# Optimization experiments

Hardware: AMD Instinct MI355X
Metric: run time of the kernel (lower is better)

## Reference

```python
import jax, jax.numpy as jnp
import numpy as np

P_SIZES = (1, 2, 4)
O_SIZE = 32
EPS = 1e-5


def bilin_matrix(S, O):
    """Interpolation matrix (O, S) for torch UpsamplingBilinear2d (align_corners=True)."""
    if S == 1:
        return jnp.ones((O, 1), dtype=jnp.float32)
    pos = jnp.arange(O, dtype=jnp.float32) * ((S - 1) / (O - 1))
    lo = jnp.clip(jnp.floor(pos).astype(jnp.int32), 0, S - 2)
    frac = pos - lo.astype(jnp.float32)
    rows = jnp.arange(O)
    M = jnp.zeros((O, S), dtype=jnp.float32)
    M = M.at[rows, lo].add(1.0 - frac).at[rows, lo + 1].add(frac)
    return M


def setup_inputs() -> dict:
    key = jax.random.key(0)
    ks = jax.random.split(key, 12)
    n, C, H = 16, 512, 32
    c4 = C // 4      # 128, value/pyramid channels
    qk = c4 // 8     # 16, query/key channels inside SAE
    s = 0.05
    return {
        "x": jax.random.normal(ks[0], (n, C, H, H), jnp.float32),
        "rce_w": jax.random.normal(ks[1], (3, c4, C), jnp.float32) * s,   # 1x1 conv per pyramid scale
        "rce_b": jax.random.normal(ks[2], (3, c4), jnp.float32) * s,
        "q_w": jax.random.normal(ks[3], (qk, c4), jnp.float32) * s,       # SAE query 1x1 conv
        "q_b": jax.random.normal(ks[4], (qk,), jnp.float32) * s,
        "k_w": jax.random.normal(ks[5], (qk, c4), jnp.float32) * s,       # SAE key 1x1 conv
        "k_b": jax.random.normal(ks[6], (qk,), jnp.float32) * s,
        "value_w": jax.random.normal(ks[7], (c4, C), jnp.float32) * s,    # value 1x1 conv
        "value_b": jax.random.normal(ks[8], (c4,), jnp.float32) * s,
        "fusion_w": jax.random.normal(ks[9], (C, 3 * c4, 3, 3), jnp.float32) * s,  # 3x3 conv, no bias
        "bn_scale": 1.0 + jax.random.normal(ks[10], (C,), jnp.float32) * s,
        "bn_bias": jax.random.normal(ks[11], (C,), jnp.float32) * s,
        "gamma": jnp.asarray(0.5, jnp.float32),
    }


def reference(x, rce_w, rce_b, q_w, q_b, k_w, k_b, value_w, value_b,
              fusion_w, bn_scale, bn_bias, gamma):
    n, C, H, W = x.shape
    c4 = C // 4
    L = H * W

    # value projection: 1x1 conv then flatten -> (n, c4, L)
    proj_value = (jnp.einsum('oc,nchw->nohw', value_w, x)
                  + value_b[None, :, None, None]).reshape(n, c4, L)

    outs = []
    for i, sz in enumerate(P_SIZES):
        # AdaptiveAvgPool2d((sz, sz)) with divisible input -> exact uniform pooling
        pooled = x.reshape(n, C, sz, H // sz, sz, W // sz).mean(axis=(3, 5))
        # 1x1 conv C -> c4
        feat = jnp.einsum('oc,ncij->noij', rce_w[i], pooled) + rce_b[i][None, :, None, None]
        # bilinear upsample (align_corners=True) to (O_SIZE, O_SIZE)
        M = bilin_matrix(sz, O_SIZE)
        up = jnp.einsum('oi,pj,ncij->ncop', M, M, feat)  # (n, c4, H, W)
        # SAE: query/key 1x1 convs, flatten, bmm + softmax
        q = (jnp.einsum('oc,nchw->nohw', q_w, up) + q_b[None, :, None, None]).reshape(n, -1, L)
        k = (jnp.einsum('oc,nchw->nohw', k_w, up) + k_b[None, :, None, None]).reshape(n, -1, L)
        energy = jnp.einsum('ncl,ncm->nlm', q, k)        # (n, L, L)
        attn = jax.nn.softmax(energy, axis=-1)
        # temp = bmm(value, attn^T): temp[c,m] = sum_l value[c,l] * attn[m,l]
        outs.append(jnp.einsum('ncl,nml->ncm', proj_value, attn).reshape(n, c4, H, W))

    cat = jnp.concatenate(outs, axis=1)                  # (n, 3*c4, H, W)
    y = jax.lax.conv_general_dilated(
        cat, fusion_w, window_strides=(1, 1), padding=((1, 1), (1, 1)),
        dimension_numbers=('NCHW', 'OIHW', 'NCHW'))
    # BatchNorm2d in training mode (default): batch statistics over (N, H, W)
    mean = y.mean(axis=(0, 2, 3))
    var = y.var(axis=(0, 2, 3))
    y = (y - mean[None, :, None, None]) * (bn_scale / jnp.sqrt(var + EPS))[None, :, None, None] \
        + bn_bias[None, :, None, None]
    y = jax.nn.relu(y)
    return gamma * y + x
```

## Files before the change

### kernel.cpp

```cpp
#include <hip/hip_runtime.h>
#include <hip/hip_fp16.h>
#include <math.h>

#define OFF_COR   0u
#define OFF_PVH   2097152u
#define OFF_Y     3145728u
#define OFF_CATP  11534336u
#define OFF_QH    15085568u
#define OFF_KH    15347712u
#define OFF_POOL  16134144u
#define OFF_FEAT  16297984u
#define OFF_AW    16338944u
#define OFF_MEANS 17223680u
#define OFF_STAT  17225728u
#define OFF_VWH   17226752u

typedef __bf16 bf16x8 __attribute__((ext_vector_type(8)));
typedef _Float16 f16x8 __attribute__((ext_vector_type(8)));
typedef _Float16 f16x4 __attribute__((ext_vector_type(4)));
typedef float f32x4 __attribute__((ext_vector_type(4)));

__device__ __forceinline__ unsigned short f2bf(float f) {
  unsigned int u = __float_as_uint(f);
  unsigned int r = u + 0x7fff + ((u >> 16) & 1);
  return (unsigned short)(r >> 16);
}

__device__ __forceinline__ unsigned short f2h(float f) {
  union { _Float16 h; unsigned short u; } cv;
  cv.h = (_Float16)f;
  return cv.u;
}

__device__ __forceinline__ void gload_lds16(const void* g, void* l) {
  __builtin_amdgcn_global_load_lds(
      (const __attribute__((address_space(1))) unsigned int*)g,
      (__attribute__((address_space(3))) unsigned int*)l, 16, 0, 0);
}

__global__ __launch_bounds__(256) void pool_kernel(const float* __restrict__ x,
                                                   float* __restrict__ pool) {
  int b = blockIdx.x;
  int t = threadIdx.x;
  const float4* xp = (const float4*)(x + (size_t)b * 1024);
  float4 v = xp[t];
  float s4 = v.x + v.y + v.z + v.w;
  __shared__ float sm[256];
  __shared__ float p4s[16];
  sm[t] = s4;
  __syncthreads();
  if (t < 16) {
    int br = t >> 2, bc = t & 3;
    float s = 0.f;
#pragma unroll
    for (int rr = 0; rr < 8; ++rr) {
      int base = br * 64 + rr * 8 + bc * 2;
      s += sm[base] + sm[base + 1];
    }
    s *= (1.f / 64.f);
    p4s[t] = s;
    pool[(size_t)b * 20 + t] = s;
  }
  __syncthreads();
  if (t < 4) {
    int i2 = t >> 1, j2 = t & 1;
    float s = (p4s[(2*i2)*4 + 2*j2]     + p4s[(2*i2)*4 + 2*j2 + 1] +
               p4s[(2*i2+1)*4 + 2*j2]   + p4s[(2*i2+1)*4 + 2*j2 + 1]) * 0.25f;
    pool[(size_t)b * 20 + 16 + t] = s;
  }
}

__global__ __launch_bounds__(64) void feat_kernel(const float* __restrict__ pool,
                                                  const float* __restrict__ rce_w,
                                                  const float* __restrict__ rce_b,
                                                  float* __restrict__ feat) {
  int o = blockIdx.x, n = blockIdx.y, t = threadIdx.x;
  float part[20];
#pragma unroll
  for (int j = 0; j < 20; ++j) part[j] = 0.f;
  for (int c = t; c < 512; c += 64) {
    const float* pl = pool + ((size_t)n * 512 + c) * 20;
    float w2 = rce_w[(size_t)(128 + o) * 512 + c];
    float w4 = rce_w[(size_t)(256 + o) * 512 + c];
#pragma unroll
    for (int j = 0; j < 4; ++j)  part[j]     += w2 * pl[16 + j];
#pragma unroll
    for (int j = 0; j < 16; ++j) part[4 + j] += w4 * pl[j];
  }
  __shared__ float red[64][20];
#pragma unroll
  for (int j = 0; j < 20; ++j) red[t][j] = part[j];
  __syncthreads();
  if (t < 20) {
    float s = 0.f;
    for (int i = 0; i < 64; ++i) s += red[i][t];
    s += (t < 4) ? rce_b[128 + o] : rce_b[256 + o];
    feat[((size_t)n * 128 + o) * 20 + t] = s;
  }
}

__global__ __launch_bounds__(256) void qk2_kernel(const float* __restrict__ feat,
                                                  const float* __restrict__ q_w,
                                                  const float* __restrict__ q_b,
                                                  const float* __restrict__ k_w,
                                                  const float* __restrict__ k_b,
                                                  unsigned short* __restrict__ qh,
                                                  unsigned short* __restrict__ kh) {
  int n = blockIdx.x, t = threadIdx.x;
  __shared__ float fL[128 * 20];
  __shared__ float GH[2][16][20];
  for (int idx = t; idx < 2560; idx += 256) fL[idx] = feat[(size_t)n * 2560 + idx];
  __syncthreads();
  for (int idx = t; idx < 640; idx += 256) {
    int which = idx / 320, rem = idx % 320, qc = rem / 20, j = rem % 20;
    const float* w = which ? k_w : q_w;
    float s = which ? k_b[qc] : q_b[qc];
    for (int c = 0; c < 128; ++c) s += w[qc * 128 + c] * fL[c * 20 + j];
    GH[which][qc][j] = s;
  }
  __syncthreads();
  for (int it = blockIdx.y * 2; it < blockIdx.y * 2 + 2; ++it) {
    int row = t + 256 * it;
    int l = row & 1023, which = (row >> 10) & 1, s = row >> 11;
    int ry = l >> 5, cx = l & 31;
    int t0, t1, t2, t3;
    float w0, w1, w2, w3;
    if (s == 0) {
      float a = ry * (1.0f / 31.0f), b = cx * (1.0f / 31.0f);
      t0 = 0; t1 = 1; t2 = 2; t3 = 3;
      w0 = (1.f - a) * (1.f - b); w1 = (1.f - a) * b;
      w2 = a * (1.f - b);         w3 = a * b;
    } else {
      float pr = ry * (3.0f / 31.0f);
      int lr = (int)pr; if (lr > 2) lr = 2;
      float fr = pr - (float)lr;
      float pc = cx * (3.0f / 31.0f);
      int lc = (int)pc; if (lc > 2) lc = 2;
      float fc = pc - (float)lc;
      int base = 4 + lr * 4 + lc;
      t0 = base; t1 = base + 1; t2 = base + 4; t3 = base + 5;
      w0 = (1.f - fr) * (1.f - fc); w1 = (1.f - fr) * fc;
      w2 = fr * (1.f - fc);         w3 = fr * fc;
    }
    float val[16];
#pragma unroll
    for (int qc = 0; qc < 16; ++qc) {
      const float* G = GH[which][qc];
      val[qc] = w0 * G[t0] + w1 * G[t1] + w2 * G[t2] + w3 * G[t3];
    }
    unsigned short* dst = (which ? kh : qh) + (((size_t)(s * 16 + n) * 1024 + l) * 16);
#pragma unroll
    for (int u = 0; u < 4; ++u)
      *(ushort4*)(dst + 4 * u) = make_ushort4(f2h(val[4*u]), f2h(val[4*u+1]),
                                              f2h(val[4*u+2]), f2h(val[4*u+3]));
  }
}

__global__ __launch_bounds__(256) void xcast_kernel(const float* __restrict__ x,
                                                    unsigned short* __restrict__ xT) {
  int lt = blockIdx.x, ct = blockIdx.y, n = blockIdx.z;
  int l0 = lt * 64, c0 = ct * 64, t = threadIdx.x;
  __shared__ float tile[64 * 65];
#pragma unroll
  for (int i = 0; i < 16; ++i) {
    int idx = t + 256 * i;
    int c = idx >> 6, l = idx & 63;
    tile[c * 65 + l] = x[((size_t)n * 512 + c0 + c) * 1024 + l0 + l];
  }
  __syncthreads();
#pragma unroll
  for (int i = 0; i < 16; ++i) {
    int idx = t + 256 * i;
    int l = idx >> 6, c = idx & 63;
    xT[((size_t)n * 1024 + l0 + l) * 512 + c0 + c] = f2h(tile[c * 65 + l]);
  }
}

__global__ __launch_bounds__(256) void prep_kernel(const float* __restrict__ fw,
                                                   const float* __restrict__ vw,
                                                   unsigned short* __restrict__ Aw,
                                                   unsigned short* __restrict__ vwh,
                                                   unsigned short* __restrict__ catp) {
  int b = blockIdx.x, t = threadIdx.x;
  if (b < 512) {
    int oc = b;
    for (int j = t; j < 2304; j += 256) {
      int seg = j >> 8, ic2 = j & 255;
      Aw[(size_t)oc * 2304 + j] = f2bf(fw[(size_t)oc * 3456 + (128 + ic2) * 9 + seg]);
    }
  } else if (b < 768) {
    int i = (b - 512) * 256 + t;
    vwh[i] = f2h(vw[i]);
  } else {
    int e = (b - 768) * 2 + (t >> 7);
    int n = e / 132, r = e % 132;
    int py, px;
    if (r < 34)       { py = 0;           px = r; }
    else if (r < 68)  { py = 33;          px = r - 34; }
    else if (r < 100) { py = r - 68 + 1;  px = 0; }
    else              { py = r - 100 + 1; px = 33; }
    unsigned int* row = (unsigned int*)(catp + ((size_t)n * 1156 + py * 34 + px) * 256);
    row[t & 127] = 0u;
  }
}

__global__ __launch_bounds__(256) void pvmm2_kernel(const unsigned short* __restrict__ vwh,
                                                    const unsigned short* __restrict__ xT,
                                                    const float* __restrict__ vb,
                                                    unsigned short* __restrict__ pvh) {
  int l0 = blockIdx.x * 64;
  int n = blockIdx.y;
  int t = threadIdx.x, lane = t & 63, wv = t >> 6;
  int wm = (wv & 1) * 64, wn = (wv >> 1) * 32;

  __shared__ short Asm[2 * 2 * 128 * 32];
  __shared__ short Bsm[2 * 2 * 64 * 32];

  int ar0 = t >> 2,        aq0 = (t & 3) ^ ((ar0 >> 1) & 3);
  int idx1 = t + 256; int ar1 = idx1 >> 2, aq1 = (idx1 & 3) ^ ((ar1 >> 1) & 3);
  int br  = t >> 2,        bq  = (t & 3) ^ ((br >> 1) & 3);
  const unsigned short* Ab0 = vwh + (size_t)ar0 * 512 + aq0 * 8;
  const unsigned short* Ab1 = vwh + (size_t)ar1 * 512 + aq1 * 8;
  const unsigned short* Bb  = xT + ((size_t)n * 1024 + l0 + br) * 512 + bq * 8;
  char* ldsA = (char*)Asm;
  char* ldsB = (char*)Bsm;
  int wvoff = wv * 1024;
  int r15 = lane & 15, kg = lane >> 4;
  int kq = kg ^ ((r15 >> 1) & 3);

  f32x4 acc[4][2];
#pragma unroll
  for (int i = 0; i < 4; ++i)
#pragma unroll
    for (int j = 0; j < 2; ++j) acc[i][j] = (f32x4){0.f, 0.f, 0.f, 0.f};

#define PV_STAGE(s, la, lb) do {                          \
    int k0_ = (s) * 64;                                   \
    gload_lds16(Ab0 + k0_,      (la) + wvoff);            \
    gload_lds16(Ab1 + k0_,      (la) + 4096 + wvoff);     \
    gload_lds16(Ab0 + k0_ + 32, (la) + 8192 + wvoff);     \
    gload_lds16(Ab1 + k0_ + 32, (la) + 12288 + wvoff);    \
    gload_lds16(Bb + k0_,       (lb) + wvoff);            \
    gload_lds16(Bb + k0_ + 32,  (lb) + 4096 + wvoff);     \
  } while (0)

  PV_STAGE(0, ldsA, ldsB);
  __syncthreads();

#pragma unroll 2
  for (int s = 0; s < 8; ++s) {
    char* la = ldsA + (s & 1) * 16384;
    char* lb = ldsB + (s & 1) * 8192;
    if (s < 7)
      PV_STAGE(s + 1, ldsA + ((s + 1) & 1) * 16384, ldsB + ((s + 1) & 1) * 8192);
#pragma unroll
    for (int c = 0; c < 2; ++c) {
      const short* As_ = (const short*)(la + c * 8192);
      const short* Bs_ = (const short*)(lb + c * 4096);
      f16x8 af[4], bfr[2];
#pragma unroll
      for (int mt2 = 0; mt2 < 4; ++mt2)
        af[mt2] = *(const f16x8*)&As_[(wm + mt2 * 16 + r15) * 32 + kq * 8];
#pragma unroll
      for (int nt2 = 0; nt2 < 2; ++nt2)
        bfr[nt2] = *(const f16x8*)&Bs_[(wn + nt2 * 16 + r15) * 32 + kq * 8];
#pragma unroll
      for (int mt2 = 0; mt2 < 4; ++mt2)
#pragma unroll
        for (int nt2 = 0; nt2 < 2; ++nt2)
          acc[mt2][nt2] = __builtin_amdgcn_mfma_f32_16x16x32_f16(af[mt2], bfr[nt2], acc[mt2][nt2], 0, 0, 0);
    }
    __syncthreads();
  }
#undef PV_STAGE

  int c_lo = wm + (lane >> 4) * 4;
  int l_lo = wn + (lane & 15);
#pragma unroll
  for (int mt2 = 0; mt2 < 4; ++mt2)
#pragma unroll
    for (int nt2 = 0; nt2 < 2; ++nt2) {
      int l = l0 + l_lo + nt2 * 16;
#pragma unroll
      for (int r = 0; r < 4; ++r) {
        int c = c_lo + mt2 * 16 + r;
        pvh[((size_t)n * 128 + c) * 1024 + l] = f2h(acc[mt2][nt2][r] + vb[c]);
      }
    }
}

__global__ __launch_bounds__(256) void mean_kernel(const unsigned short* __restrict__ pvh,
                                                   float* __restrict__ means) {
  int c = blockIdx.x, n = blockIdx.y, t = threadIdx.x;
  f16x4 v = ((const f16x4*)(pvh + ((size_t)n * 128 + c) * 1024))[t];
  float s = (float)v[0] + (float)v[1] + (float)v[2] + (float)v[3];
  for (int o = 32; o > 0; o >>= 1) s += __shfl_down(s, o);
  __shared__ float wsum[4];
  if ((t & 63) == 0) wsum[t >> 6] = s;
  __syncthreads();
  if (t == 0) means[n * 128 + c] = (wsum[0] + wsum[1] + wsum[2] + wsum[3]) * (1.f / 1024.f);
}

__global__ __launch_bounds__(64) void basecor_kernel(const float* __restrict__ means,
                                                     const float* __restrict__ fw,
                                                     float* __restrict__ cor) {
  int oc = blockIdx.x, n = blockIdx.y, t = threadIdx.x;
  float S[9];
#pragma unroll
  for (int j = 0; j < 9; ++j) S[j] = 0.f;
  for (int c = t; c < 128; c += 64) {
    float m = means[n * 128 + c];
    const float* wp = fw + (size_t)oc * 3456 + c * 9;
#pragma unroll
    for (int j = 0; j < 9; ++j) S[j] += m * wp[j];
  }
  __shared__ float red[64][9];
  __shared__ float Sf[9];
#pragma unroll
  for (int j = 0; j < 9; ++j) red[t][j] = S[j];
  __syncthreads();
  if (t < 9) {
    float s = 0.f;
    for (int i = 0; i < 64; ++i) s += red[i][t];
    Sf[t] = s;
  }
  __syncthreads();
  if (t < 9) {
    int a = t / 3, b = t % 3;
    float s = 0.f;
#pragma unroll
    for (int ky = 0; ky < 3; ++ky) {
      if ((a == 0 && ky == 0) || (a == 2 && ky == 2)) continue;
#pragma unroll
      for (int kx = 0; kx < 3; ++kx) {
        if ((b == 0 && kx == 0) || (b == 2 && kx == 2)) continue;
        s += Sf[ky * 3 + kx];
      }
    }
    cor[((size_t)n * 512 + oc) * 9 + t] = s;
  }
}

__global__ __launch_bounds__(256) void fattn_kernel(const unsigned short* __restrict__ qh,
                                                    const unsigned short* __restrict__ kh,
                                                    const unsigned short* __restrict__ pvh,
                                                    unsigned short* __restrict__ catp) {
  int m0 = blockIdx.x * 64;
  int n = blockIdx.y, sc = blockIdx.z;
  int t = threadIdx.x, lane = t & 63, wv = t >> 6;
  int wc = (wv >> 1) * 64;
  int wm2 = (wv & 1) * 32;
  int r15 = lane & 15, kg = lane >> 4;
  int kq = kg ^ ((r15 >> 1) & 3);

  const unsigned short* qb  = qh + ((size_t)(sc * 16 + n) * 1024 + m0 + wv * 16) * 16;
  const unsigned short* kb  = kh + ((size_t)(sc * 16 + n) * 1024) * 16;
  const unsigned short* pvb = pvh + (size_t)n * 128 * 1024;

  __shared__ short PVs[2 * 2 * 128 * 32];
  __shared__ _Float16 Us[64 * 72];
  __shared__ float rsum[64];

  f16x8 zf = {0, 0, 0, 0, 0, 0, 0, 0};
  f16x8 qa = (kg < 2) ? *(const f16x8*)(qb + r15 * 16 + kg * 8) : zf;

  int prow = t >> 2;
  int aq = (t & 3) ^ ((prow >> 1) & 3);
  const unsigned short* Pb0 = pvb + (size_t)prow * 1024 + aq * 8;
  const unsigned short* Pb1 = pvb + (size_t)(prow + 64) * 1024 + aq * 8;
  char* ldsPV = (char*)PVs;
  int wvoff = wv * 1024;

  f32x4 acc[4][2];
#pragma unroll
  for (int i = 0; i < 4; ++i)
#pragma unroll
    for (int j = 0; j < 2; ++j) acc[i][j] = (f32x4){0.f, 0.f, 0.f, 0.f};
  float rs[4] = {0.f, 0.f, 0.f, 0.f};

  gload_lds16(Pb0,      ldsPV + wvoff);
  gload_lds16(Pb1,      ldsPV + 4096 + wvoff);
  gload_lds16(Pb0 + 32, ldsPV + 8192 + wvoff);
  gload_lds16(Pb1 + 32, ldsPV + 12288 + wvoff);

  for (int it = 0; it < 16; ++it) {
    int cur = it & 1;
    int l0 = it * 64;
    f16x8 kbf[4];
#pragma unroll
    for (int lt = 0; lt < 4; ++lt)
      kbf[lt] = (kg < 2)
        ? *(const f16x8*)(kb + (size_t)(l0 + lt * 16 + r15) * 16 + kg * 8) : zf;
    if (it < 15) {
      char* dst = ldsPV + (cur ^ 1) * 16384 + wvoff;
      gload_lds16(Pb0 + l0 + 64, dst);
      gload_lds16(Pb1 + l0 + 64, dst + 4096);
      gload_lds16(Pb0 + l0 + 96, dst + 8192);
      gload_lds16(Pb1 + l0 + 96, dst + 12288);
    }
    f32x4 sacc[4];
#pragma unroll
    for (int lt = 0; lt < 4; ++lt)
      sacc[lt] = __builtin_amdgcn_mfma_f32_16x16x32_f16(qa, kbf[lt], (f32x4){0.f,0.f,0.f,0.f}, 0, 0, 0);
#pragma unroll
    for (int lt = 0; lt < 4; ++lt)
#pragma unroll
      for (int r = 0; r < 4; ++r) {
        float e = __expf(sacc[lt][r]);
        Us[(wv * 16 + kg * 4 + r) * 72 + lt * 16 + r15] = (_Float16)e;
        rs[r] += e;
      }
    asm volatile("s_waitcnt vmcnt(4) lgkmcnt(0)" ::: "memory");
    __builtin_amdgcn_s_barrier();
    __builtin_amdgcn_sched_barrier(0);
#pragma unroll
    for (int ks = 0; ks < 2; ++ks) {
      f16x8 bfr[2];
#pragma unroll
      for (int nt = 0; nt < 2; ++nt)
        bfr[nt] = *(const f16x8*)&Us[(wm2 + nt * 16 + r15) * 72 + ks * 32 + kg * 8];
#pragma unroll
      for (int ct = 0; ct < 4; ++ct) {
        f16x8 af = *(const f16x8*)&PVs[cur * 8192 + ks * 4096 + (wc + ct * 16 + r15) * 32 + kq * 8];
#pragma unroll
        for (int nt = 0; nt < 2; ++nt)
          acc[ct][nt] = __builtin_amdgcn_mfma_f32_16x16x32_f16(af, bfr[nt], acc[ct][nt], 0, 0, 0);
      }
    }
    asm volatile("s_waitcnt lgkmcnt(0)" ::: "memory");
    __builtin_amdgcn_s_barrier();
    __builtin_amdgcn_sched_barrier(0);
  }

#pragma unroll
  for (int r = 0; r < 4; ++r) {
    rs[r] += __shfl_xor(rs[r], 1);
    rs[r] += __shfl_xor(rs[r], 2);
    rs[r] += __shfl_xor(rs[r], 4);
    rs[r] += __shfl_xor(rs[r], 8);
  }
  if (r15 == 0) {
#pragma unroll
    for (int r = 0; r < 4; ++r) rsum[wv * 16 + kg * 4 + r] = rs[r];
  }
  __syncthreads();

#pragma unroll
  for (int nt = 0; nt < 2; ++nt) {
    float inv = 1.f / rsum[wm2 + nt * 16 + r15];
    int pix = m0 + wm2 + nt * 16 + r15;
    unsigned short* ob = catp + ((size_t)n * 1156 + ((pix >> 5) + 1) * 34 + (pix & 31) + 1) * 256
                       + sc * 128 + wc + kg * 4;
#pragma unroll
    for (int ct = 0; ct < 4; ++ct) {
      ushort4 o = make_ushort4(f2bf(acc[ct][nt][0] * inv), f2bf(acc[ct][nt][1] * inv),
                               f2bf(acc[ct][nt][2] * inv), f2bf(acc[ct][nt][3] * inv));
      *(ushort4*)(ob + ct * 16) = o;
    }
  }
}

__device__ __forceinline__ void conv_stage(const unsigned short* __restrict__ Aw,
                                           const unsigned short* __restrict__ catp,
                                           size_t abase0, size_t abase1,
                                           size_t bbase0, size_t bbase1,
                                           int s, char* la, char* lb, int wvoff) {
  int seg = s >> 2;
  size_t akk  = (size_t)s * 64;
  size_t boff = (size_t)((seg / 3) * 34 + (seg % 3)) * 256 + (size_t)(s & 3) * 64;
  gload_lds16(Aw + abase0 + akk,          la + wvoff);
  gload_lds16(Aw + abase1 + akk,          la + 4096 + wvoff);
  gload_lds16(Aw + abase0 + akk + 32,     la + 8192 + wvoff);
  gload_lds16(Aw + abase1 + akk + 32,     la + 12288 + wvoff);
  gload_lds16(catp + bbase0 + boff,       lb + wvoff);
  gload_lds16(catp + bbase1 + boff,       lb + 4096 + wvoff);
  gload_lds16(catp + bbase0 + boff + 32,  lb + 8192 + wvoff);
  gload_lds16(catp + bbase1 + boff + 32,  lb + 12288 + wvoff);
}

__device__ __forceinline__ void conv_comp(const short* As_, const short* Bs_,
                                          int wm, int wn, int r15, int kq,
                                          f32x4 acc[4][4]) {
  bf16x8 af[4], bf[4];
#pragma unroll
  for (int mt = 0; mt < 4; ++mt)
    af[mt] = *(const bf16x8*)&As_[(wm + mt * 16 + r15) * 32 + kq * 8];
#pragma unroll
  for (int nt = 0; nt < 4; ++nt)
    bf[nt] = *(const bf16x8*)&Bs_[(wn + nt * 16 + r15) * 32 + kq * 8];
#pragma unroll
  for (int mt = 0; mt < 4; ++mt)
#pragma unroll
    for (int nt = 0; nt < 4; ++nt)
      acc[mt][nt] = __builtin_amdgcn_mfma_f32_16x16x32_bf16(af[mt], bf[nt], acc[mt][nt], 0, 0, 0);
}

__global__ __launch_bounds__(256) void convmm_kernel(const unsigned short* __restrict__ Aw,
                                                     const unsigned short* __restrict__ catp,
                                                     const float* __restrict__ cor,
                                                     float* __restrict__ y) {
  int ntile = blockIdx.x;
  int n = ntile >> 3, y0 = (ntile & 7) * 4;
  int m0 = blockIdx.y * 128;
  int t = threadIdx.x;
  int lane = t & 63, wv = t >> 6;
  int wm = (wv & 1) * 64, wn = (wv >> 1) * 64;

  __shared__ short Asm[2 * 2 * 128 * 32];
  __shared__ short Bsm[2 * 2 * 128 * 32];

  int idx0 = t, idx1 = t + 256;
  int ar0 = idx0 >> 2, aq0 = (idx0 & 3) ^ ((ar0 >> 1) & 3);
  int ar1 = idx1 >> 2, aq1 = (idx1 & 3) ^ ((ar1 >> 1) & 3);
  size_t abase0 = (size_t)(m0 + ar0) * 2304 + aq0 * 8;
  size_t abase1 = (size_t)(m0 + ar1) * 2304 + aq1 * 8;
  size_t bbase0 = ((size_t)n * 1156 + (size_t)(y0 + (ar0 >> 5)) * 34 + (ar0 & 31)) * 256 + aq0 * 8;
  size_t bbase1 = ((size_t)n * 1156 + (size_t)(y0 + (ar1 >> 5)) * 34 + (ar1 & 31)) * 256 + aq1 * 8;
  char* ldsA = (char*)Asm;
  char* ldsB = (char*)Bsm;
  int wvoff = wv * 1024;

  int r15 = lane & 15, kg = lane >> 4;
  int kq = kg ^ ((r15 >> 1) & 3);

  f32x4 acc[4][4];
#pragma unroll
  for (int i = 0; i < 4; ++i)
#pragma unroll
    for (int j = 0; j < 4; ++j) acc[i][j] = (f32x4){0.f, 0.f, 0.f, 0.f};

  conv_stage(Aw, catp, abase0, abase1, bbase0, bbase1, 0, ldsA, ldsB, wvoff);
  __syncthreads();

#pragma unroll 2
  for (int s = 0; s < 36; ++s) {
    char* la = ldsA + (s & 1) * 16384;
    char* lb = ldsB + (s & 1) * 16384;
    if (s < 35)
      conv_stage(Aw, catp, abase0, abase1, bbase0, bbase1, s + 1,
                 ldsA + ((s + 1) & 1) * 16384, ldsB + ((s + 1) & 1) * 16384, wvoff);
    conv_comp((const short*)la,          (const short*)lb,          wm, wn, r15, kq, acc);
    conv_comp((const short*)(la + 8192), (const short*)(lb + 8192), wm, wn, r15, kq, acc);
    __syncthreads();
  }

  int pixbase = (ntile & 7) * 128 + wn + (lane & 15);
  int ocbase = m0 + wm + (lane >> 4) * 4;
#pragma unroll
  for (int mt = 0; mt < 4; ++mt)
#pragma unroll
    for (int nt = 0; nt < 4; ++nt) {
      int oc = ocbase + mt * 16;
      int pix = pixbase + nt * 16;
      int py = pix >> 5, px = pix & 31;
      int yc = (py == 0) ? 0 : ((py == 31) ? 2 : 1);
      int xc = (px == 0) ? 0 : ((px == 31) ? 2 : 1);
      const float* cp = cor + ((size_t)n * 512 + oc) * 9 + yc * 3 + xc;
      float* yp = y + ((size_t)n * 512 + oc) * 1024 + pix;
#pragma unroll
      for (int r = 0; r < 4; ++r) yp[(size_t)r * 1024] = acc[mt][nt][r] + cp[(size_t)r * 9];
    }
}

__global__ __launch_bounds__(256) void bnstat_kernel(const float* __restrict__ y,
                                                     const float* __restrict__ bn_scale,
                                                     const float* __restrict__ bn_bias,
                                                     float* __restrict__ stats) {
  int oc = blockIdx.x, t = threadIdx.x;
  float s = 0.f, ss = 0.f;
  for (int n = 0; n < 16; ++n) {
    float4 v = ((const float4*)(y + ((size_t)n * 512 + oc) * 1024))[t];
    s  += v.x + v.y + v.z + v.w;
    ss += v.x * v.x + v.y * v.y + v.z * v.z + v.w * v.w;
  }
  for (int o = 32; o > 0; o >>= 1) {
    s  += __shfl_down(s, o);
    ss += __shfl_down(ss, o);
  }
  __shared__ float rs[4], rss[4];
  if ((t & 63) == 0) { rs[t >> 6] = s; rss[t >> 6] = ss; }
  __syncthreads();
  if (t == 0) {
    float S = rs[0] + rs[1] + rs[2] + rs[3];
    float SS = rss[0] + rss[1] + rss[2] + rss[3];
    float mean = S * (1.f / 16384.f);
    float var = SS * (1.f / 16384.f) - mean * mean;
    float se = bn_scale[oc] / sqrtf(var + 1e-5f);
    stats[oc * 2] = se;
    stats[oc * 2 + 1] = bn_bias[oc] - mean * se;
  }
}

__global__ __launch_bounds__(256) void final_kernel(const float* __restrict__ y,
                                                    const float* __restrict__ x,
                                                    const float* __restrict__ stats,
                                                    const float* __restrict__ gamma,
                                                    float* __restrict__ outp) {
  int b = blockIdx.x;
  int c = b & 511;
  int t = threadIdx.x;
  float se = stats[c * 2], sh = stats[c * 2 + 1], g = gamma[0];
  float4 yv = ((const float4*)(y + (size_t)b * 1024))[t];
  float4 xv = ((const float4*)(x + (size_t)b * 1024))[t];
  float4 o;
  o.x = g * fmaxf(yv.x * se + sh, 0.f) + xv.x;
  o.y = g * fmaxf(yv.y * se + sh, 0.f) + xv.y;
  o.z = g * fmaxf(yv.z * se + sh, 0.f) + xv.z;
  o.w = g * fmaxf(yv.w * se + sh, 0.f) + xv.w;
  ((float4*)(outp + (size_t)b * 1024))[t] = o;
}

extern "C" void kernel_launch(void* const* d_in, const int* in_sizes, int n_in,
                              void* d_out, int out_size, void* d_ws, size_t ws_size,
                              hipStream_t stream) {
  const float* x        = (const float*)d_in[0];
  const float* rce_w    = (const float*)d_in[1];
  const float* rce_b    = (const float*)d_in[2];
  const float* q_w      = (const float*)d_in[3];
  const float* q_b      = (const float*)d_in[4];
  const float* k_w      = (const float*)d_in[5];
  const float* k_b      = (const float*)d_in[6];
  const float* value_w  = (const float*)d_in[7];
  const float* value_b  = (const float*)d_in[8];
  const float* fw       = (const float*)d_in[9];
  const float* bn_scale = (const float*)d_in[10];
  const float* bn_bias  = (const float*)d_in[11];
  const float* gamma    = (const float*)d_in[12];

  float* ws    = (float*)d_ws;
  float* cor   = ws + OFF_COR;
  unsigned short* pvh = (unsigned short*)(ws + OFF_PVH);
  float* ybuf  = ws + OFF_Y;
  unsigned short* xTbuf = (unsigned short*)(ws + OFF_Y);
  unsigned short* catp = (unsigned short*)(ws + OFF_CATP);
  unsigned short* qh   = (unsigned short*)(ws + OFF_QH);
  unsigned short* kh   = (unsigned short*)(ws + OFF_KH);
  float* pool  = ws + OFF_POOL;
  float* feat  = ws + OFF_FEAT;
  unsigned short* Aw = (unsigned short*)(ws + OFF_AW);
  float* means = ws + OFF_MEANS;
  float* stats = ws + OFF_STAT;
  unsigned short* vwh = (unsigned short*)(ws + OFF_VWH);
  float* outp  = (float*)d_out;

  hipLaunchKernelGGL(pool_kernel,    dim3(8192),       dim3(256), 0, stream, x, pool);
  hipLaunchKernelGGL(feat_kernel,    dim3(128, 16),    dim3(64),  0, stream, pool, rce_w, rce_b, feat);
  hipLaunchKernelGGL(qk2_kernel,     dim3(16, 8),      dim3(256), 0, stream, feat, q_w, q_b, k_w, k_b, qh, kh);
  hipLaunchKernelGGL(xcast_kernel,   dim3(16, 8, 16),  dim3(256), 0, stream, x, xTbuf);
  hipLaunchKernelGGL(prep_kernel,    dim3(1824),       dim3(256), 0, stream, fw, value_w, Aw, vwh, catp);
  hipLaunchKernelGGL(pvmm2_kernel,   dim3(16, 16),     dim3(256), 0, stream, vwh, xTbuf, value_b, pvh);
  hipLaunchKernelGGL(mean_kernel,    dim3(128, 16),    dim3(256), 0, stream, pvh, means);
  hipLaunchKernelGGL(basecor_kernel, dim3(512, 16),    dim3(64),  0, stream, means, fw, cor);
  hipLaunchKernelGGL(fattn_kernel,   dim3(16, 16, 2),  dim3(256), 0, stream, qh, kh, pvh, catp);
  hipLaunchKernelGGL(convmm_kernel,  dim3(128, 4),     dim3(256), 0, stream, Aw, catp, cor, ybuf);
  hipLaunchKernelGGL(bnstat_kernel,  dim3(512),        dim3(256), 0, stream, ybuf, bn_scale, bn_bias, stats);
  hipLaunchKernelGGL(final_kernel,   dim3(8192),       dim3(256), 0, stream, ybuf, x, stats, gamma, outp);
}
```

Measured before the change: 243.3 us.

## Fuse pooling into xcast and BN statistics into conv epilogue

Removes the separate pool kernel by computing 4x4 average pools with shuffles and atomics inside the transpose/cast kernel, deriving the 2x2 pool in feat_kernel, and zeroing the pool buffer in prep_kernel, which now runs first. The convolution epilogue also reduces per-channel sum and sum of squares into a partials buffer, so bnstat reads 128 partials per channel instead of re-reading the whole y tensor. This saves two full passes over large tensors. The cost is atomics in xcast, extra shuffles and an LDS reduction in the conv epilogue, and a launch-order dependency on pool zeroing.

Measured after the change: 243.4 us. About the same (+0.1%).

```diff
diff --git a/kernel.cpp b/kernel.cpp
--- a/kernel.cpp
+++ b/kernel.cpp
@@ -3,12 +3,13 @@
 #include <math.h>
 
 #define OFF_COR   0u
+#define OFF_PART  131072u
+#define OFF_P4    262144u
 #define OFF_PVH   2097152u
 #define OFF_Y     3145728u
 #define OFF_CATP  11534336u
 #define OFF_QH    15085568u
 #define OFF_KH    15347712u
-#define OFF_POOL  16134144u
 #define OFF_FEAT  16297984u
 #define OFF_AW    16338944u
 #define OFF_MEANS 17223680u
@@ -38,39 +39,7 @@
       (__attribute__((address_space(3))) unsigned int*)l, 16, 0, 0);
 }
 
-__global__ __launch_bounds__(256) void pool_kernel(const float* __restrict__ x,
-                                                   float* __restrict__ pool) {
-  int b = blockIdx.x;
-  int t = threadIdx.x;
-  const float4* xp = (const float4*)(x + (size_t)b * 1024);
-  float4 v = xp[t];
-  float s4 = v.x + v.y + v.z + v.w;
-  __shared__ float sm[256];
-  __shared__ float p4s[16];
-  sm[t] = s4;
-  __syncthreads();
-  if (t < 16) {
-    int br = t >> 2, bc = t & 3;
-    float s = 0.f;
-#pragma unroll
-    for (int rr = 0; rr < 8; ++rr) {
-      int base = br * 64 + rr * 8 + bc * 2;
-      s += sm[base] + sm[base + 1];
-    }
-    s *= (1.f / 64.f);
-    p4s[t] = s;
-    pool[(size_t)b * 20 + t] = s;
-  }
-  __syncthreads();
-  if (t < 4) {
-    int i2 = t >> 1, j2 = t & 1;
-    float s = (p4s[(2*i2)*4 + 2*j2]     + p4s[(2*i2)*4 + 2*j2 + 1] +
-               p4s[(2*i2+1)*4 + 2*j2]   + p4s[(2*i2+1)*4 + 2*j2 + 1]) * 0.25f;
-    pool[(size_t)b * 20 + 16 + t] = s;
-  }
-}
-
-__global__ __launch_bounds__(64) void feat_kernel(const float* __restrict__ pool,
+__global__ __launch_bounds__(64) void feat_kernel(const float* __restrict__ pool4,
                                                   const float* __restrict__ rce_w,
                                                   const float* __restrict__ rce_b,
                                                   float* __restrict__ feat) {
@@ -79,11 +48,16 @@
 #pragma unroll
   for (int j = 0; j < 20; ++j) part[j] = 0.f;
   for (int c = t; c < 512; c += 64) {
-    const float* pl = pool + ((size_t)n * 512 + c) * 20;
+    const float* pl = pool4 + ((size_t)n * 512 + c) * 16;
     float w2 = rce_w[(size_t)(128 + o) * 512 + c];
     float w4 = rce_w[(size_t)(256 + o) * 512 + c];
 #pragma unroll
-    for (int j = 0; j < 4; ++j)  part[j]     += w2 * pl[16 + j];
+    for (int j = 0; j < 4; ++j) {
+      int i2 = j >> 1, j2 = j & 1;
+      float p2 = 0.25f * (pl[(2 * i2) * 4 + 2 * j2]     + pl[(2 * i2) * 4 + 2 * j2 + 1] +
+                          pl[(2 * i2 + 1) * 4 + 2 * j2] + pl[(2 * i2 + 1) * 4 + 2 * j2 + 1]);
+      part[j] += w2 * p2;
+    }
 #pragma unroll
     for (int j = 0; j < 16; ++j) part[4 + j] += w4 * pl[j];
   }
@@ -157,15 +131,26 @@
 }
 
 __global__ __launch_bounds__(256) void xcast_kernel(const float* __restrict__ x,
-                                                    unsigned short* __restrict__ xT) {
+                                                    unsigned short* __restrict__ xT,
+                                                    float* __restrict__ pool4) {
   int lt = blockIdx.x, ct = blockIdx.y, n = blockIdx.z;
   int l0 = lt * 64, c0 = ct * 64, t = threadIdx.x;
+  int br4 = (lt >> 2) * 4;
   __shared__ float tile[64 * 65];
 #pragma unroll
   for (int i = 0; i < 16; ++i) {
     int idx = t + 256 * i;
-    int c = idx >> 6, l = idx & 63;
-    tile[c * 65 + l] = x[((size_t)n * 512 + c0 + c) * 1024 + l0 + l];
+    int cl = idx >> 6, l = idx & 63;
+    float v = x[((size_t)n * 512 + c0 + cl) * 1024 + l0 + l];
+    tile[cl * 65 + l] = v;
+    float pv = v;
+    pv += __shfl_xor(pv, 32);
+    pv += __shfl_xor(pv, 1);
+    pv += __shfl_xor(pv, 2);
+    pv += __shfl_xor(pv, 4);
+    if ((l & 39) == 0)
+      atomicAdd(&pool4[((size_t)n * 512 + c0 + cl) * 16 + br4 + (l >> 3)],
+                pv * (1.f / 64.f));
   }
   __syncthreads();
 #pragma unroll
@@ -180,7 +165,8 @@
                                                    const float* __restrict__ vw,
                                                    unsigned short* __restrict__ Aw,
                                                    unsigned short* __restrict__ vwh,
-                                                   unsigned short* __restrict__ catp) {
+                                                   unsigned short* __restrict__ catp,
+                                                   float* __restrict__ pool4) {
   int b = blockIdx.x, t = threadIdx.x;
   if (b < 512) {
     int oc = b;
@@ -191,7 +177,7 @@
   } else if (b < 768) {
     int i = (b - 512) * 256 + t;
     vwh[i] = f2h(vw[i]);
-  } else {
+  } else if (b < 1824) {
     int e = (b - 768) * 2 + (t >> 7);
     int n = e / 132, r = e % 132;
     int py, px;
@@ -201,6 +187,9 @@
     else              { py = r - 100 + 1; px = 33; }
     unsigned int* row = (unsigned int*)(catp + ((size_t)n * 1156 + py * 34 + px) * 256);
     row[t & 127] = 0u;
+  } else {
+    int i = (b - 1824) * 1024 + t * 4;
+    *(float4*)(pool4 + i) = make_float4(0.f, 0.f, 0.f, 0.f);
   }
 }
 
@@ -498,7 +487,8 @@
 __global__ __launch_bounds__(256) void convmm_kernel(const unsigned short* __restrict__ Aw,
                                                      const unsigned short* __restrict__ catp,
                                                      const float* __restrict__ cor,
-                                                     float* __restrict__ y) {
+                                                     float* __restrict__ y,
+                                                     float* __restrict__ part) {
   int ntile = blockIdx.x;
   int n = ntile >> 3, y0 = (ntile & 7) * 4;
   int m0 = blockIdx.y * 128;
@@ -546,6 +536,9 @@
 
   int pixbase = (ntile & 7) * 128 + wn + (lane & 15);
   int ocbase = m0 + wm + (lane >> 4) * 4;
+  float sloc[16], ssloc[16];
+#pragma unroll
+  for (int id = 0; id < 16; ++id) { sloc[id] = 0.f; ssloc[id] = 0.f; }
 #pragma unroll
   for (int mt = 0; mt < 4; ++mt)
 #pragma unroll
@@ -558,31 +551,59 @@
       const float* cp = cor + ((size_t)n * 512 + oc) * 9 + yc * 3 + xc;
       float* yp = y + ((size_t)n * 512 + oc) * 1024 + pix;
 #pragma unroll
-      for (int r = 0; r < 4; ++r) yp[(size_t)r * 1024] = acc[mt][nt][r] + cp[(size_t)r * 9];
-    }
-}
-
-__global__ __launch_bounds__(256) void bnstat_kernel(const float* __restrict__ y,
+      for (int r = 0; r < 4; ++r) {
+        float yv = acc[mt][nt][r] + cp[(size_t)r * 9];
+        yp[(size_t)r * 1024] = yv;
+        sloc[mt * 4 + r]  += yv;
+        ssloc[mt * 4 + r] += yv * yv;
+      }
+    }
+#pragma unroll
+  for (int id = 0; id < 16; ++id) {
+#pragma unroll
+    for (int o = 8; o > 0; o >>= 1) {
+      sloc[id]  += __shfl_xor(sloc[id], o);
+      ssloc[id] += __shfl_xor(ssloc[id], o);
+    }
+  }
+  float* ps = (float*)Bsm;
+  if (r15 == 0) {
+#pragma unroll
+    for (int id = 0; id < 16; ++id) {
+      ps[((wv * 4 + kg) * 16 + id) * 2]     = sloc[id];
+      ps[((wv * 4 + kg) * 16 + id) * 2 + 1] = ssloc[id];
+    }
+  }
+  __syncthreads();
+  {
+    int ocl = t >> 1, stat = t & 1;
+    int wmh = ocl >> 6, rem = ocl & 63;
+    int mt = rem >> 4, kgg = (rem >> 2) & 3, r = rem & 3, id = mt * 4 + r;
+    float val = ps[((wmh * 4 + kgg) * 16 + id) * 2 + stat]
+              + ps[(((wmh + 2) * 4 + kgg) * 16 + id) * 2 + stat];
+    part[((size_t)(blockIdx.y * 128 + ocl) * 2 + stat) * 128 + ntile] = val;
+  }
+}
+
+__global__ __launch_bounds__(128) void bnstat_kernel(const float* __restrict__ part,
                                                      const float* __restrict__ bn_scale,
                                                      const float* __restrict__ bn_bias,
                                                      float* __restrict__ stats) {
   int oc = blockIdx.x, t = threadIdx.x;
-  float s = 0.f, ss = 0.f;
-  for (int n = 0; n < 16; ++n) {
-    float4 v = ((const float4*)(y + ((size_t)n * 512 + oc) * 1024))[t];
-    s  += v.x + v.y + v.z + v.w;
-    ss += v.x * v.x + v.y * v.y + v.z * v.z + v.w * v.w;
-  }
+  int mt = oc >> 7, ocl = oc & 127;
+  const float* sb = part + ((size_t)(mt * 128 + ocl) * 2 + 0) * 128;
+  const float* qb = part + ((size_t)(mt * 128 + ocl) * 2 + 1) * 128;
+  float s = sb[t], ss = qb[t];
   for (int o = 32; o > 0; o >>= 1) {
     s  += __shfl_down(s, o);
     ss += __shfl_down(ss, o);
   }
-  __shared__ float rs[4], rss[4];
-  if ((t & 63) == 0) { rs[t >> 6] = s; rss[t >> 6] = ss; }
+  __shared__ float r0[2], r1[2];
+  if ((t & 63) == 0) { r0[t >> 6] = s; r1[t >> 6] = ss; }
   __syncthreads();
   if (t == 0) {
-    float S = rs[0] + rs[1] + rs[2] + rs[3];
-    float SS = rss[0] + rss[1] + rss[2] + rss[3];
+    float S = r0[0] + r0[1];
+    float SS = r1[0] + r1[1];
     float mean = S * (1.f / 16384.f);
     float var = SS * (1.f / 16384.f) - mean * mean;
     float se = bn_scale[oc] / sqrtf(var + 1e-5f);
@@ -629,13 +650,14 @@
 
   float* ws    = (float*)d_ws;
   float* cor   = ws + OFF_COR;
+  float* part  = ws + OFF_PART;
+  float* pool4 = ws + OFF_P4;
   unsigned short* pvh = (unsigned short*)(ws + OFF_PVH);
   float* ybuf  = ws + OFF_Y;
   unsigned short* xTbuf = (unsigned short*)(ws + OFF_Y);
   unsigned short* catp = (unsigned short*)(ws + OFF_CATP);
   unsigned short* qh   = (unsigned short*)(ws + OFF_QH);
   unsigned short* kh   = (unsigned short*)(ws + OFF_KH);
-  float* pool  = ws + OFF_POOL;
   float* feat  = ws + OFF_FEAT;
   unsigned short* Aw = (unsigned short*)(ws + OFF_AW);
   float* means = ws + OFF_MEANS;
@@ -643,16 +665,15 @@
   unsigned short* vwh = (unsigned short*)(ws + OFF_VWH);
   float* outp  = (float*)d_out;
 
-  hipLaunchKernelGGL(pool_kernel,    dim3(8192),       dim3(256), 0, stream, x, pool);
-  hipLaunchKernelGGL(feat_kernel,    dim3(128, 16),    dim3(64),  0, stream, pool, rce_w, rce_b, feat);
+  hipLaunchKernelGGL(prep_kernel,    dim3(1952),       dim3(256), 0, stream, fw, value_w, Aw, vwh, catp, pool4);
+  hipLaunchKernelGGL(xcast_kernel,   dim3(16, 8, 16),  dim3(256), 0, stream, x, xTbuf, pool4);
+  hipLaunchKernelGGL(feat_kernel,    dim3(128, 16),    dim3(64),  0, stream, pool4, rce_w, rce_b, feat);
   hipLaunchKernelGGL(qk2_kernel,     dim3(16, 8),      dim3(256), 0, stream, feat, q_w, q_b, k_w, k_b, qh, kh);
-  hipLaunchKernelGGL(xcast_kernel,   dim3(16, 8, 16),  dim3(256), 0, stream, x, xTbuf);
-  hipLaunchKernelGGL(prep_kernel,    dim3(1824),       dim3(256), 0, stream, fw, value_w, Aw, vwh, catp);
   hipLaunchKernelGGL(pvmm2_kernel,   dim3(16, 16),     dim3(256), 0, stream, vwh, xTbuf, value_b, pvh);
   hipLaunchKernelGGL(mean_kernel,    dim3(128, 16),    dim3(256), 0, stream, pvh, means);
   hipLaunchKernelGGL(basecor_kernel, dim3(512, 16),    dim3(64),  0, stream, means, fw, cor);
   hipLaunchKernelGGL(fattn_kernel,   dim3(16, 16, 2),  dim3(256), 0, stream, qh, kh, pvh, catp);
-  hipLaunchKernelGGL(convmm_kernel,  dim3(128, 4),     dim3(256), 0, stream, Aw, catp, cor, ybuf);
-  hipLaunchKernelGGL(bnstat_kernel,  dim3(512),        dim3(256), 0, stream, ybuf, bn_scale, bn_bias, stats);
+  hipLaunchKernelGGL(convmm_kernel,  dim3(128, 4),     dim3(256), 0, stream, Aw, catp, cor, ybuf, part);
+  hipLaunchKernelGGL(bnstat_kernel,  dim3(512),        dim3(128), 0, stream, part, bn_scale, bn_bias, stats);
   hipLaunchKernelGGL(final_kernel,   dim3(8192),       dim3(256), 0, stream, ybuf, x, stats, gamma, outp);
 }
```
